# Kernel optimization log

Measured on AMD Instinct MI355X. Metric: run time of the kernel, lower is better.

## Reference

```python
import jax, jax.numpy as jnp
import numpy as np

EPS = 1e-12  # matches torch F.normalize eps

def _l2_normalize(x):
    n = jnp.linalg.norm(x, axis=-1, keepdims=True)
    return x / jnp.maximum(n, EPS)

def setup_inputs() -> dict:
    key = jax.random.key(0)
    k1, k2, k3 = jax.random.split(key, 3)
    B, D, C = 2048, 1024, 65536
    return {
        "query": jax.random.normal(k1, (B, D), dtype=jnp.float32),
        "memory_keys": jax.random.normal(k2, (C, D), dtype=jnp.float32),
        "memory_values": jax.random.normal(k3, (C, D), dtype=jnp.float32),
        "memory_usage": jnp.zeros((C,), dtype=jnp.float32),
        "k": 8,
    }

def reference(query, memory_keys, memory_values, memory_usage, k):
    # cosine similarity: [B, C]
    qn = _l2_normalize(query)
    mn = _l2_normalize(memory_keys)
    sims = jnp.matmul(qn, mn.T)
    # top-k indices per query: [B, k]
    _, indices = jax.lax.top_k(sims, k)
    # gather retrieved keys/values: [B, k, D]
    retrieved_keys = memory_keys[indices]
    retrieved_values = memory_values[indices]
    # usage scatter-add (+1 per retrieved slot), vectorized form of the loop
    capacity = memory_usage.shape[0]
    counts = jax.ops.segment_sum(
        jnp.ones(indices.size, dtype=memory_usage.dtype),
        indices.reshape(-1),
        num_segments=capacity,
    )
    usage_new = memory_usage + counts
    return retrieved_keys, retrieved_values, usage_new
```

## Files before the change

### kernel.cpp

```cpp
#include <hip/hip_runtime.h>
#include <math.h>

#define BQ 2048
#define DD 1024
#define CC 65536
#define KSEL 8
#define NSTRIPE 32
#define SC (CC / NSTRIPE)
#define GTM 128
#define GTN 128
#define GBK 32
#define NTILES (SC / GTN)
#define LCAND 8
#define TRES 32

typedef unsigned int u32;
typedef unsigned short ushort_t;
typedef __attribute__((ext_vector_type(8))) short bf16x8;
typedef __attribute__((ext_vector_type(4))) float f32x4;


#define FENCE() asm volatile("" ::: "memory")
#define LGKM0() asm volatile("s_waitcnt lgkmcnt(0)" ::: "memory")

__device__ __forceinline__ ushort_t f2bf(float f) {
    u32 u = __builtin_bit_cast(u32, f);
    return (ushort_t)((u + 0x7FFFu + ((u >> 16) & 1u)) >> 16);
}

__device__ __forceinline__ void gl_lds16(const ushort_t* g, ushort_t* l) {
    __builtin_amdgcn_global_load_lds(
        (const __attribute__((address_space(1))) u32*)g,
        (__attribute__((address_space(3))) u32*)l, 16, 0, 0);
}

__global__ __launch_bounds__(256) void normconv_kernel(
    const float* __restrict__ q, const float* __restrict__ keys,
    double* __restrict__ qinv, double* __restrict__ kinv,
    ushort_t* __restrict__ qn, ushort_t* __restrict__ kn)
{
    __shared__ double red[4];
    const int row = blockIdx.x;
    const int t = threadIdx.x;
    const bool iskey = row < CC;
    const float* src = iskey ? keys + (size_t)row * DD
                             : q + (size_t)(row - CC) * DD;
    float4 v = ((const float4*)src)[t];
    double s = (double)v.x * v.x + (double)v.y * v.y +
               (double)v.z * v.z + (double)v.w * v.w;
    for (int off = 32; off > 0; off >>= 1) s += __shfl_down(s, off);
    if ((t & 63) == 0) red[t >> 6] = s;
    __syncthreads();
    const double tot = red[0] + red[1] + red[2] + red[3];
    const double inv = 1.0 / fmax(sqrt(tot), 1e-12);
    if (t == 0) {
        if (iskey) kinv[row] = inv; else qinv[row - CC] = inv;
    }
    const float invf = (float)inv;
    ushort4 o;
    o.x = f2bf(v.x * invf); o.y = f2bf(v.y * invf);
    o.z = f2bf(v.z * invf); o.w = f2bf(v.w * invf);
    ushort_t* dst = iskey ? kn + (size_t)row * DD
                          : qn + (size_t)(row - CC) * DD;
    ((ushort4*)dst)[t] = o;
}

__global__ __launch_bounds__(256, 3) void gemm_topk_kernel(
    const ushort_t* __restrict__ qn, const ushort_t* __restrict__ kn,
    unsigned* __restrict__ cand)
{
    __shared__ ushort_t As[2][GTM * GBK];
    __shared__ ushort_t Bs[2][GTN * GBK];
    __shared__ float tilebuf[GTM][33];

    const int tid = threadIdx.x;
    const int wid = tid >> 6;
    const int lane = tid & 63;
    const int wy = wid >> 1, wx = wid & 1;
    const int l15 = lane & 15, quad = lane >> 4;

    const int flat = blockIdx.y * 16 + blockIdx.x;
    const int swz  = (flat & 7) * 64 + (flat >> 3);
    const int bx = swz & 15, by = swz >> 4;
    const int m0 = bx * GTM;
    const int sbase = by * SC;

    const int e0 = tid, e1 = tid + 256;
    const int ks0 = (((e0 & 3) ^ ((e0 >> 3) & 3)) * 8);
    const int ks1 = (((e1 & 3) ^ ((e1 >> 3) & 3)) * 8);
    const ushort_t* gA0 = qn + (size_t)(m0 + (e0 >> 2)) * DD + ks0;
    const ushort_t* gA1 = qn + (size_t)(m0 + (e1 >> 2)) * DD + ks1;
    const ushort_t* gB0 = kn + (size_t)(sbase + (e0 >> 2)) * DD + ks0;
    const ushort_t* gB1 = kn + (size_t)(sbase + (e1 >> 2)) * DD + ks1;

#define STAGE(buf, k0_) do {                         \
        gl_lds16(gA0 + (k0_), As[buf] + e0 * 8);     \
        gl_lds16(gA1 + (k0_), As[buf] + e1 * 8);     \
        gl_lds16(gB0 + (k0_), Bs[buf] + e0 * 8);     \
        gl_lds16(gB1 + (k0_), Bs[buf] + e1 * 8);     \
    } while (0)

    float tv[LCAND];
    int ti[LCAND];
#pragma unroll
    for (int l = 0; l < LCAND; ++l) { tv[l] = -3.0e38f; ti[l] = 0; }
    float minv = -3.0e38f;
    int minpos = 0;

    const int swz15 = (l15 >> 1) & 3;

    STAGE(0, 0);

    for (int nt = 0; nt < NTILES; ++nt) {
        const int cbase = sbase + nt * GTN;

        f32x4 acc[4][4];
#pragma unroll
        for (int i = 0; i < 4; ++i)
#pragma unroll
            for (int j = 0; j < 4; ++j) acc[i][j] = (f32x4)0.0f;

#pragma unroll 2
        for (int kt = 0; kt < DD / GBK; ++kt) {
            const int cur = kt & 1;
            if (kt < DD / GBK - 1) {
                STAGE(cur ^ 1, (kt + 1) * GBK);
                asm volatile("s_waitcnt vmcnt(4)" ::: "memory");
            } else if (nt < NTILES - 1) {
                gB0 += (size_t)GTN * DD;
                gB1 += (size_t)GTN * DD;
                STAGE(cur ^ 1, 0);
                asm volatile("s_waitcnt vmcnt(4)" ::: "memory");
            } else {
                asm volatile("s_waitcnt vmcnt(0)" ::: "memory");
            }
            __builtin_amdgcn_s_barrier();
            FENCE();
            __builtin_amdgcn_s_setprio(1);

            bf16x8 af[4], bfr[4];
#pragma unroll
            for (int ri = 0; ri < 4; ++ri)
                af[ri] = *(const bf16x8*)(As[cur] +
                    (wy * 64 + ri * 16 + l15) * GBK + ((quad ^ swz15) * 8));
#pragma unroll
            for (int ci = 0; ci < 4; ++ci)
                bfr[ci] = *(const bf16x8*)(Bs[cur] +
                    (wx * 64 + ci * 16 + l15) * GBK + ((quad ^ swz15) * 8));
#pragma unroll
            for (int ri = 0; ri < 4; ++ri)
#pragma unroll
                for (int ci = 0; ci < 4; ++ci)
                    acc[ri][ci] = __builtin_amdgcn_mfma_f32_16x16x32_bf16(
                        af[ri], bfr[ci], acc[ri][ci], 0, 0, 0);

            __builtin_amdgcn_s_setprio(0);
            FENCE();
            __builtin_amdgcn_s_barrier();
            FENCE();
        }

        for (int c4 = 0; c4 < 4; ++c4) {
            LGKM0();
            __builtin_amdgcn_s_barrier();
            FENCE();
            if (wx == (c4 >> 1)) {
                const int cilo = (c4 & 1) * 2;
#pragma unroll
                for (int ri = 0; ri < 4; ++ri)
#pragma unroll
                    for (int cx = 0; cx < 2; ++cx)
#pragma unroll
                        for (int r = 0; r < 4; ++r)
                            tilebuf[wy * 64 + ri * 16 + quad * 4 + r][cx * 16 + l15] =
                                acc[ri][cilo + cx][r];
            }
            LGKM0();
            __builtin_amdgcn_s_barrier();
            FENCE();
            {
                const int rr = tid & 127;
                const int jb = (tid >> 7) << 4;
                const int gc0 = cbase + c4 * 32 + jb;
                for (int j = 0; j < 16; ++j) {
                    float v = tilebuf[rr][jb + j];
                    if (v > minv) {
                        tv[minpos] = v; ti[minpos] = gc0 + j;
                        minv = tv[0]; minpos = 0;
#pragma unroll
                        for (int l = 1; l < LCAND; ++l)
                            if (tv[l] < minv) { minv = tv[l]; minpos = l; }
                    }
                }
            }
        }
    }

    LGKM0();
    __builtin_amdgcn_s_barrier();
    FENCE();
    if (tid >= 128) {
        const int r2 = tid - 128;
#pragma unroll
        for (int l = 0; l < LCAND; ++l) {
            tilebuf[r2][l] = tv[l];
            tilebuf[r2][16 + l] = __int_as_float(ti[l]);
        }
    }
    LGKM0();
    __builtin_amdgcn_s_barrier();
    FENCE();
    if (tid < GTM) {
#pragma unroll
        for (int c = 0; c < LCAND; ++c) {
            float v = tilebuf[tid][c];
            int idx = __float_as_int(tilebuf[tid][16 + c]);
            if (v > minv) {
                tv[minpos] = v; ti[minpos] = idx;
                minv = tv[0]; minpos = 0;
#pragma unroll
                for (int l = 1; l < LCAND; ++l)
                    if (tv[l] < minv) { minv = tv[l]; minpos = l; }
            }
        }
        unsigned* dst = cand + (size_t)(m0 + tid) * (NSTRIPE * LCAND) + by * LCAND;
#pragma unroll
        for (int l = 0; l < LCAND; ++l)
            dst[l] = ((unsigned)f2bf(tv[l]) << 16) | (unsigned)(ti[l] & 0xFFFF);
    }
#undef STAGE
}

__global__ __launch_bounds__(256) void merge_kernel(
    const int* __restrict__ cand, int* __restrict__ sel_idx,
    float* __restrict__ counts)
{
    const int gid = blockIdx.x * 256 + threadIdx.x;
    if (gid < CC) counts[gid] = 0.0f;
    const int row = gid >> 6;
    const int lane = threadIdx.x & 63;
    const int* cv = cand + (size_t)row * (NSTRIPE * LCAND);
    int v[4];
#pragma unroll
    for (int u = 0; u < 4; ++u) v[u] = cv[lane + 64 * u];
    for (int r = 0; r < TRES; ++r) {
        int bv = v[0];
#pragma unroll
        for (int u = 1; u < 4; ++u) bv = max(bv, v[u]);
#pragma unroll
        for (int off = 1; off < 64; off <<= 1) bv = max(bv, __shfl_xor(bv, off));
#pragma unroll
        for (int u = 0; u < 4; ++u)
            if (v[u] == bv) v[u] = (int)0x80000000;
        if (lane == 0) sel_idx[row * TRES + r] = bv & 0xFFFF;
    }
}

__global__ __launch_bounds__(256) void rescore_kernel(
    const float* __restrict__ q, const float* __restrict__ keys,
    const double* __restrict__ qinv, const double* __restrict__ kinv,
    const int* __restrict__ sel_idx, double* __restrict__ sel_val)
{
    __shared__ float qs[DD];
    const int b = blockIdx.x;
    const int t = threadIdx.x;
    ((float4*)qs)[t] = ((const float4*)(q + (size_t)b * DD))[t];
    __syncthreads();
    const int wv = t >> 6, lane = t & 63;
    const double qi = qinv[b];
    for (int cc = wv; cc < TRES; cc += 4) {
        const int c = sel_idx[b * TRES + cc];
        const float4* kr = (const float4*)(keys + (size_t)c * DD);
        double s = 0.0;
#pragma unroll
        for (int u = 0; u < 4; ++u) {
            float4 a = ((const float4*)qs)[lane + 64 * u];
            float4 k4 = kr[lane + 64 * u];
            s += (double)a.x * k4.x + (double)a.y * k4.y +
                 (double)a.z * k4.z + (double)a.w * k4.w;
        }
        for (int off = 32; off > 0; off >>= 1) s += __shfl_down(s, off);
        if (lane == 0) sel_val[b * TRES + cc] = s * qi * kinv[c];
    }
}

__global__ __launch_bounds__(256) void finalize_kernel(
    const double* __restrict__ sel_val, const int* __restrict__ sel_idx,
    int* __restrict__ topk_idx, float* __restrict__ counts)
{
    const int b = blockIdx.x * 256 + threadIdx.x;
    if (b >= BQ) return;
    double bv[KSEL]; int bi[KSEL];
#pragma unroll
    for (int j = 0; j < KSEL; ++j) { bv[j] = -1.0e300; bi[j] = 0x7fffffff; }
    for (int t = 0; t < TRES; ++t) {
        double v = sel_val[b * TRES + t];
        int idx = sel_idx[b * TRES + t];
        int p = KSEL;
        while (p > 0 && (v > bv[p - 1] || (v == bv[p - 1] && idx < bi[p - 1]))) --p;
        if (p < KSEL) {
            for (int s = KSEL - 1; s > p; --s) { bv[s] = bv[s - 1]; bi[s] = bi[s - 1]; }
            bv[p] = v; bi[p] = idx;
        }
    }
    for (int j = 0; j < KSEL; ++j) {
        topk_idx[b * KSEL + j] = bi[j];
        atomicAdd(&counts[bi[j]], 1.0f);
    }
}

__global__ __launch_bounds__(256) void gather_kernel(
    const float* __restrict__ keys, const float* __restrict__ values,
    const int* __restrict__ topk_idx, float* __restrict__ out_k,
    float* __restrict__ out_v)
{
    const int pair = blockIdx.x;
    const int c = topk_idx[pair];
    const int t = threadIdx.x;
    const float4* ks = (const float4*)(keys + (size_t)c * DD);
    const float4* vs = (const float4*)(values + (size_t)c * DD);
    float4* ok = (float4*)out_k + (size_t)pair * (DD / 4);
    float4* ov = (float4*)out_v + (size_t)pair * (DD / 4);
    ok[t] = ks[t];
    ov[t] = vs[t];
}

__global__ __launch_bounds__(256) void usage_kernel(
    const float* __restrict__ usage_in, const float* __restrict__ counts,
    float* __restrict__ out_u)
{
    const int c = blockIdx.x * 256 + threadIdx.x;
    out_u[c] = usage_in[c] + counts[c];
}

extern "C" void kernel_launch(void* const* d_in, const int* in_sizes, int n_in,
                              void* d_out, int out_size, void* d_ws, size_t ws_size,
                              hipStream_t stream)
{
    const float* q      = (const float*)d_in[0];
    const float* keys   = (const float*)d_in[1];
    const float* values = (const float*)d_in[2];
    const float* usage  = (const float*)d_in[3];

    char* ws = (char*)d_ws;
    double* qinv     = (double*)(ws + 0);
    double* kinv     = (double*)(ws + 16384);
    ushort_t* qn     = (ushort_t*)(ws + 540672);
    float* counts    = (float*)(ws + 540672);
    int* sel_idx     = (int*)(ws + 802816);
    double* sel_val  = (double*)(ws + 1064960);
    int* topk        = (int*)(ws + 1589248);
    unsigned* cand   = (unsigned*)(ws + 4734976);

    float* out_k = (float*)d_out;
    float* out_v = out_k + (size_t)BQ * KSEL * DD;
    float* out_u = out_v + (size_t)BQ * KSEL * DD;
    ushort_t* kn = (ushort_t*)d_out;

    normconv_kernel<<<CC + BQ, 256, 0, stream>>>(q, keys, qinv, kinv, qn, kn);

    dim3 g2(BQ / GTM, NSTRIPE);
    gemm_topk_kernel<<<g2, 256, 0, stream>>>(qn, kn, cand);

    merge_kernel<<<BQ / 4, 256, 0, stream>>>((const int*)cand, sel_idx, counts);

    rescore_kernel<<<BQ, 256, 0, stream>>>(q, keys, qinv, kinv, sel_idx, sel_val);

    finalize_kernel<<<BQ / 256, 256, 0, stream>>>(sel_val, sel_idx, topk, counts);

    gather_kernel<<<BQ * KSEL, 256, 0, stream>>>(keys, values, topk, out_k, out_v);

    usage_kernel<<<CC / 256, 256, 0, stream>>>(usage, counts, out_u);
}
```

Before: 1.133 ms.

## Enlarge GEMM-topk tile to 256x256 with 512-thread blocks

Doubles the fused GEMM+top-k block tile from 128x128 to 256x256 and the block size from 256 to 512 threads. Eight waves are laid out 2x4, and each wave now computes 128x64 with an 8x4 MFMA accumulator grid. The goal is higher arithmetic intensity: fewer global/LDS loads per FLOP and fewer blocks streaming the key matrix. In exchange the grid shrinks to 256 blocks, which is near one wave of blocks on the GPU, and register pressure and LDS per block go up. The per-tile top-k extraction now takes 8 column chunks instead of 4, each with two barriers.

```diff
diff --git a/kernel.cpp b/kernel.cpp
--- a/kernel.cpp
+++ b/kernel.cpp
@@ -7,10 +7,10 @@
 #define KSEL 8
 #define NSTRIPE 32
 #define SC (CC / NSTRIPE)
-#define GTM 128
-#define GTN 128
+#define BM2 256
+#define BN2 256
 #define GBK 32
-#define NTILES (SC / GTN)
+#define NTILES2 (SC / BN2)
 #define LCAND 8
 #define TRES 32
 
@@ -65,39 +65,37 @@
     ((ushort4*)dst)[t] = o;
 }
 
-__global__ __launch_bounds__(256, 3) void gemm_topk_kernel(
+__global__ __launch_bounds__(512, 2) void gemm_topk_kernel(
     const ushort_t* __restrict__ qn, const ushort_t* __restrict__ kn,
     unsigned* __restrict__ cand)
 {
-    __shared__ ushort_t As[2][GTM * GBK];
-    __shared__ ushort_t Bs[2][GTN * GBK];
-    __shared__ float tilebuf[GTM][33];
-
-    const int tid = threadIdx.x;
-    const int wid = tid >> 6;
-    const int lane = tid & 63;
-    const int wy = wid >> 1, wx = wid & 1;
+    __shared__ ushort_t As[2][BM2 * GBK];
+    __shared__ ushort_t Bs[2][BN2 * GBK];
+    __shared__ float tilebuf[BM2][33];
+
+    const int t = threadIdx.x;
+    const int wid = t >> 6;
+    const int lane = t & 63;
+    const int wy = wid >> 2, wx = wid & 3;
     const int l15 = lane & 15, quad = lane >> 4;
 
-    const int flat = blockIdx.y * 16 + blockIdx.x;
-    const int swz  = (flat & 7) * 64 + (flat >> 3);
-    const int bx = swz & 15, by = swz >> 4;
-    const int m0 = bx * GTM;
+    const int flat = blockIdx.y * 8 + blockIdx.x;
+    const int swz  = (flat & 7) * 32 + (flat >> 3);
+    const int bx = swz & 7, by = swz >> 3;
+    const int m0 = bx * BM2;
     const int sbase = by * SC;
 
-    const int e0 = tid, e1 = tid + 256;
-    const int ks0 = (((e0 & 3) ^ ((e0 >> 3) & 3)) * 8);
-    const int ks1 = (((e1 & 3) ^ ((e1 >> 3) & 3)) * 8);
-    const ushort_t* gA0 = qn + (size_t)(m0 + (e0 >> 2)) * DD + ks0;
-    const ushort_t* gA1 = qn + (size_t)(m0 + (e1 >> 2)) * DD + ks1;
-    const ushort_t* gB0 = kn + (size_t)(sbase + (e0 >> 2)) * DD + ks0;
-    const ushort_t* gB1 = kn + (size_t)(sbase + (e1 >> 2)) * DD + ks1;
-
-#define STAGE(buf, k0_) do {                         \
-        gl_lds16(gA0 + (k0_), As[buf] + e0 * 8);     \
-        gl_lds16(gA1 + (k0_), As[buf] + e1 * 8);     \
-        gl_lds16(gB0 + (k0_), Bs[buf] + e0 * 8);     \
-        gl_lds16(gB1 + (k0_), Bs[buf] + e1 * 8);     \
+    const int ks = (((t & 3) ^ ((t >> 3) & 3)) * 8);
+    const ushort_t* gA0 = qn + (size_t)(m0 + (t >> 2)) * DD + ks;
+    const ushort_t* gA1 = gA0 + (size_t)128 * DD;
+    const ushort_t* gB0 = kn + (size_t)(sbase + (t >> 2)) * DD + ks;
+    const ushort_t* gB1 = gB0 + (size_t)128 * DD;
+
+#define STAGE(buf, k0_) do {                              \
+        gl_lds16(gA0 + (k0_), As[buf] + t * 8);           \
+        gl_lds16(gA1 + (k0_), As[buf] + (t + 512) * 8);   \
+        gl_lds16(gB0 + (k0_), Bs[buf] + t * 8);           \
+        gl_lds16(gB1 + (k0_), Bs[buf] + (t + 512) * 8);   \
     } while (0)
 
     float tv[LCAND];
@@ -111,12 +109,12 @@
 
     STAGE(0, 0);
 
-    for (int nt = 0; nt < NTILES; ++nt) {
-        const int cbase = sbase + nt * GTN;
-
-        f32x4 acc[4][4];
-#pragma unroll
-        for (int i = 0; i < 4; ++i)
+    for (int nt = 0; nt < NTILES2; ++nt) {
+        const int cbase = sbase + nt * BN2;
+
+        f32x4 acc[8][4];
+#pragma unroll
+        for (int i = 0; i < 8; ++i)
 #pragma unroll
             for (int j = 0; j < 4; ++j) acc[i][j] = (f32x4)0.0f;
 
@@ -126,9 +124,9 @@
             if (kt < DD / GBK - 1) {
                 STAGE(cur ^ 1, (kt + 1) * GBK);
                 asm volatile("s_waitcnt vmcnt(4)" ::: "memory");
-            } else if (nt < NTILES - 1) {
-                gB0 += (size_t)GTN * DD;
-                gB1 += (size_t)GTN * DD;
+            } else if (nt < NTILES2 - 1) {
+                gB0 += (size_t)BN2 * DD;
+                gB1 += (size_t)BN2 * DD;
                 STAGE(cur ^ 1, 0);
                 asm volatile("s_waitcnt vmcnt(4)" ::: "memory");
             } else {
@@ -138,17 +136,17 @@
             FENCE();
             __builtin_amdgcn_s_setprio(1);
 
-            bf16x8 af[4], bfr[4];
-#pragma unroll
-            for (int ri = 0; ri < 4; ++ri)
+            bf16x8 af[8], bfr[4];
+#pragma unroll
+            for (int ri = 0; ri < 8; ++ri)
                 af[ri] = *(const bf16x8*)(As[cur] +
-                    (wy * 64 + ri * 16 + l15) * GBK + ((quad ^ swz15) * 8));
+                    (wy * 128 + ri * 16 + l15) * GBK + ((quad ^ swz15) * 8));
 #pragma unroll
             for (int ci = 0; ci < 4; ++ci)
                 bfr[ci] = *(const bf16x8*)(Bs[cur] +
                     (wx * 64 + ci * 16 + l15) * GBK + ((quad ^ swz15) * 8));
 #pragma unroll
-            for (int ri = 0; ri < 4; ++ri)
+            for (int ri = 0; ri < 8; ++ri)
 #pragma unroll
                 for (int ci = 0; ci < 4; ++ci)
                     acc[ri][ci] = __builtin_amdgcn_mfma_f32_16x16x32_bf16(
@@ -160,28 +158,29 @@
             FENCE();
         }
 
-        for (int c4 = 0; c4 < 4; ++c4) {
+#pragma unroll
+        for (int c8 = 0; c8 < 8; ++c8) {
             LGKM0();
             __builtin_amdgcn_s_barrier();
             FENCE();
-            if (wx == (c4 >> 1)) {
-                const int cilo = (c4 & 1) * 2;
-#pragma unroll
-                for (int ri = 0; ri < 4; ++ri)
+            if (wx == (c8 >> 1)) {
+                const int cilo = (c8 & 1) * 2;
+#pragma unroll
+                for (int ri = 0; ri < 8; ++ri)
 #pragma unroll
                     for (int cx = 0; cx < 2; ++cx)
 #pragma unroll
                         for (int r = 0; r < 4; ++r)
-                            tilebuf[wy * 64 + ri * 16 + quad * 4 + r][cx * 16 + l15] =
+                            tilebuf[wy * 128 + ri * 16 + quad * 4 + r][cx * 16 + l15] =
                                 acc[ri][cilo + cx][r];
             }
             LGKM0();
             __builtin_amdgcn_s_barrier();
             FENCE();
             {
-                const int rr = tid & 127;
-                const int jb = (tid >> 7) << 4;
-                const int gc0 = cbase + c4 * 32 + jb;
+                const int rr = t & 255;
+                const int jb = (t >> 8) << 4;
+                const int gc0 = cbase + c8 * 32 + jb;
                 for (int j = 0; j < 16; ++j) {
                     float v = tilebuf[rr][jb + j];
                     if (v > minv) {
@@ -199,8 +198,8 @@
     LGKM0();
     __builtin_amdgcn_s_barrier();
     FENCE();
-    if (tid >= 128) {
-        const int r2 = tid - 128;
+    if (t >= 256) {
+        const int r2 = t - 256;
 #pragma unroll
         for (int l = 0; l < LCAND; ++l) {
             tilebuf[r2][l] = tv[l];
@@ -210,11 +209,11 @@
     LGKM0();
     __builtin_amdgcn_s_barrier();
     FENCE();
-    if (tid < GTM) {
+    if (t < 256) {
 #pragma unroll
         for (int c = 0; c < LCAND; ++c) {
-            float v = tilebuf[tid][c];
-            int idx = __float_as_int(tilebuf[tid][16 + c]);
+            float v = tilebuf[t][c];
+            int idx = __float_as_int(tilebuf[t][16 + c]);
             if (v > minv) {
                 tv[minpos] = v; ti[minpos] = idx;
                 minv = tv[0]; minpos = 0;
@@ -223,7 +222,7 @@
                     if (tv[l] < minv) { minv = tv[l]; minpos = l; }
             }
         }
-        unsigned* dst = cand + (size_t)(m0 + tid) * (NSTRIPE * LCAND) + by * LCAND;
+        unsigned* dst = cand + (size_t)(m0 + t) * (NSTRIPE * LCAND) + by * LCAND;
 #pragma unroll
         for (int l = 0; l < LCAND; ++l)
             dst[l] = ((unsigned)f2bf(tv[l]) << 16) | (unsigned)(ti[l] & 0xFFFF);
@@ -359,8 +358,8 @@
 
     normconv_kernel<<<CC + BQ, 256, 0, stream>>>(q, keys, qinv, kinv, qn, kn);
 
-    dim3 g2(BQ / GTM, NSTRIPE);
-    gemm_topk_kernel<<<g2, 256, 0, stream>>>(qn, kn, cand);
+    dim3 g2(BQ / BM2, NSTRIPE);
+    gemm_topk_kernel<<<g2, 512, 0, stream>>>(qn, kn, cand);
 
     merge_kernel<<<BQ / 4, 256, 0, stream>>>((const int*)cand, sel_idx, counts);
 
```

Measured after the change: 1.045 ms. 7.7% less time.
